# Performance work log

Measured on AMD Instinct MI355X. Metric: run time of the kernel, lower is better.

The kernel has to match this reference:

```python
import jax, jax.numpy as jnp
import numpy as np

N, E, F_IN, F_HID, K = 100000, 1600000, 64, 64, 6


def setup_inputs() -> dict:
    key = jax.random.key(0)
    k1, k2, k3, k4, k5 = jax.random.split(key, 5)
    x = jax.random.normal(k1, (N, F_IN), dtype=jnp.float32)
    # edges with no self-loops (PyG ChebConv removes self loops before normalization)
    src = jax.random.randint(k2, (E,), 0, N, dtype=jnp.int32)
    off = jax.random.randint(k3, (E,), 1, N, dtype=jnp.int32)
    dst = (src + off) % N
    edge_index = jnp.stack([src, dst], axis=0)
    # Glorot-ish init for the K Chebyshev weight matrices
    W = jax.random.normal(k4, (K, F_IN, F_HID), dtype=jnp.float32) * (1.0 / np.sqrt(F_IN))
    b = jax.random.normal(k5, (F_HID,), dtype=jnp.float32) * 0.01
    return {"x": x, "edge_index": edge_index, "W": W, "b": b}


def reference(x, edge_index, W, b):
    # ChebConv with sym normalization, lambda_max = 2.0 (PyG default):
    # scaled Laplacian L_hat = 2*L/lambda_max - I = -D^{-1/2} A D^{-1/2} (zero diagonal)
    row = edge_index[0].astype(jnp.int32)  # source j
    col = edge_index[1].astype(jnp.int32)  # target i
    n = x.shape[0]
    deg = jax.ops.segment_sum(jnp.ones_like(row, dtype=x.dtype), row, num_segments=n)
    dinv = jnp.where(deg > 0, jax.lax.rsqrt(deg), jnp.zeros_like(deg))
    w = -(dinv[row] * dinv[col])  # [E] edge weights of L_hat

    def prop(h):  # h: [N, F] -> L_hat @ h via gather-scale-scatter
        return jax.ops.segment_sum(w[:, None] * h[row], col, num_segments=n)

    # Chebyshev recurrence: Tx_0 = x, Tx_1 = L_hat x, Tx_k = 2 L_hat Tx_{k-1} - Tx_{k-2}
    Tx0 = x
    out = Tx0 @ W[0]
    Tx1 = prop(Tx0)
    out = out + Tx1 @ W[1]
    for k in range(2, W.shape[0]):
        Tx2 = 2.0 * prop(Tx1) - Tx0
        out = out + Tx2 @ W[k]
        Tx0, Tx1 = Tx1, Tx2
    return jax.nn.relu(out + b)
```

## Files before the change

### kernel.cpp

```cpp
#include <hip/hip_runtime.h>


constexpr int F = 64;
constexpr int SCAN_ELEMS = 2048;
constexpr int BSH = 9;
constexpr int EPB = 2048;
constexpr int PNPW = 8;
constexpr int WFRAG_BLOCKS = 12;

typedef __attribute__((ext_vector_type(8))) short short8;
typedef __attribute__((ext_vector_type(4))) float floatx4;

__device__ __forceinline__ unsigned short f_to_bf(float f) {
    unsigned u = __float_as_uint(f);
    u += 0x7FFFu + ((u >> 16) & 1u);
    return (unsigned short)(u >> 16);
}
__device__ __forceinline__ float bf_to_f(unsigned short s) {
    return __uint_as_float(((unsigned)s) << 16);
}
__device__ __forceinline__ float4 bf4_to_f4(ushort4 u) {
    float4 f;
    f.x = bf_to_f(u.x); f.y = bf_to_f(u.y); f.z = bf_to_f(u.z); f.w = bf_to_f(u.w);
    return f;
}

__global__ void hist2_kernel(const int* __restrict__ row, const int* __restrict__ col,
                             int* __restrict__ gcH, int* __restrict__ gcS,
                             int P, int G, int E) {
    __shared__ int hH[256], hS[256];
    const int tid = threadIdx.x, blk = blockIdx.x;
    hH[tid] = 0; hS[tid] = 0;
    __syncthreads();
    const int start = blk * EPB + tid * 8;
    if (start + 7 < E) {
        const int4 c0 = *(const int4*)(col + start);
        const int4 c1 = *(const int4*)(col + start + 4);
        const int4 r0 = *(const int4*)(row + start);
        const int4 r1 = *(const int4*)(row + start + 4);
        atomicAdd(&hH[c0.x >> BSH], 1); atomicAdd(&hH[c0.y >> BSH], 1);
        atomicAdd(&hH[c0.z >> BSH], 1); atomicAdd(&hH[c0.w >> BSH], 1);
        atomicAdd(&hH[c1.x >> BSH], 1); atomicAdd(&hH[c1.y >> BSH], 1);
        atomicAdd(&hH[c1.z >> BSH], 1); atomicAdd(&hH[c1.w >> BSH], 1);
        atomicAdd(&hS[r0.x >> BSH], 1); atomicAdd(&hS[r0.y >> BSH], 1);
        atomicAdd(&hS[r0.z >> BSH], 1); atomicAdd(&hS[r0.w >> BSH], 1);
        atomicAdd(&hS[r1.x >> BSH], 1); atomicAdd(&hS[r1.y >> BSH], 1);
        atomicAdd(&hS[r1.z >> BSH], 1); atomicAdd(&hS[r1.w >> BSH], 1);
    } else {
        for (int k = start; k < E && k < start + 8; ++k) {
            atomicAdd(&hH[col[k] >> BSH], 1);
            atomicAdd(&hS[row[k] >> BSH], 1);
        }
    }
    __syncthreads();
    if (tid < P) {
        gcH[(size_t)tid * G + blk] = hH[tid];
        gcS[(size_t)tid * G + blk] = hS[tid];
    }
}

__device__ __forceinline__ int4 load_cnt4(const int* __restrict__ cnt, int i, int N) {
    int4 v = make_int4(0, 0, 0, 0);
    if (i + 3 < N) {
        v = *(const int4*)(cnt + i);
    } else {
        if (i + 0 < N) v.x = cnt[i + 0];
        if (i + 1 < N) v.y = cnt[i + 1];
        if (i + 2 < N) v.z = cnt[i + 2];
        if (i + 3 < N) v.w = cnt[i + 3];
    }
    return v;
}

__global__ void scan1_kernel(const int* __restrict__ cnt, int* __restrict__ bsum, int N) {
    const int tid = threadIdx.x;
    const int i = blockIdx.x * SCAN_ELEMS + tid * 8;
    int4 va = load_cnt4(cnt, i, N);
    int4 vb = load_cnt4(cnt, i + 4, N);
    int s = va.x + va.y + va.z + va.w + vb.x + vb.y + vb.z + vb.w;
#pragma unroll
    for (int off = 1; off < 64; off <<= 1) s += __shfl_xor(s, off);
    __shared__ int ws[4];
    if ((tid & 63) == 0) ws[tid >> 6] = s;
    __syncthreads();
    if (tid == 0) bsum[blockIdx.x] = ws[0] + ws[1] + ws[2] + ws[3];
}

__global__ void scan2_kernel(const int* __restrict__ bsum, int* __restrict__ boff,
                             int* __restrict__ total_out, int nb) {
    const int tid = threadIdx.x;
    const int lane = tid & 63, w = tid >> 6;
    int v = (tid < nb) ? bsum[tid] : 0;
    int inc = v;
#pragma unroll
    for (int off = 1; off < 64; off <<= 1) {
        int t = __shfl_up(inc, off);
        if (lane >= off) inc += t;
    }
    __shared__ int wsum[4];
    if (lane == 63) wsum[w] = inc;
    __syncthreads();
    int wo = 0;
    for (int k = 0; k < w; ++k) wo += wsum[k];
    const int excl = wo + inc - v;
    if (tid < nb) boff[tid] = excl;
    if (tid == nb - 1) *total_out = excl + v;
}

__global__ void scan3_kernel(const int* __restrict__ cnt, const int* __restrict__ boff,
                             int* __restrict__ dst, int N) {
    const int tid = threadIdx.x;
    const int lane = tid & 63, w = tid >> 6;
    const int i = blockIdx.x * SCAN_ELEMS + tid * 8;
    int4 va = load_cnt4(cnt, i, N);
    int4 vb = load_cnt4(cnt, i + 4, N);
    const int s = va.x + va.y + va.z + va.w + vb.x + vb.y + vb.z + vb.w;
    int inc = s;
#pragma unroll
    for (int off = 1; off < 64; off <<= 1) {
        int t = __shfl_up(inc, off);
        if (lane >= off) inc += t;
    }
    __shared__ int wsum[4];
    if (lane == 63) wsum[w] = inc;
    __syncthreads();
    int wo = 0;
    for (int k = 0; k < w; ++k) wo += wsum[k];
    const int r0 = boff[blockIdx.x] + wo + inc - s;
    const int r1 = r0 + va.x, r2 = r1 + va.y, r3 = r2 + va.z;
    const int r4 = r3 + va.w, r5 = r4 + vb.x, r6 = r5 + vb.y, r7 = r6 + vb.z;
    if (i + 3 < N) {
        *(int4*)(dst + i) = make_int4(r0, r1, r2, r3);
    } else {
        if (i + 0 < N) dst[i + 0] = r0;
        if (i + 1 < N) dst[i + 1] = r1;
        if (i + 2 < N) dst[i + 2] = r2;
    }
    if (i + 7 < N) {
        *(int4*)(dst + i + 4) = make_int4(r4, r5, r6, r7);
    } else {
        if (i + 4 < N) dst[i + 4] = r4;
        if (i + 5 < N) dst[i + 5] = r5;
        if (i + 6 < N) dst[i + 6] = r6;
    }
}

__global__ void part2_kernel(const int* __restrict__ row, const int* __restrict__ col,
                             const int* __restrict__ goH, const int* __restrict__ goS,
                             int* __restrict__ partH, int* __restrict__ partS,
                             int P, int G, int E) {
    __shared__ int cH[256], cS[256];
    const int tid = threadIdx.x, blk = blockIdx.x;
    if (tid < P) {
        cH[tid] = goH[(size_t)tid * G + blk];
        cS[tid] = goS[(size_t)tid * G + blk] - E;
    }
    __syncthreads();
    const int start = blk * EPB + tid * 8;
    if (start + 7 < E) {
        const int4 c0 = *(const int4*)(col + start);
        const int4 c1 = *(const int4*)(col + start + 4);
        const int4 r0 = *(const int4*)(row + start);
        const int4 r1 = *(const int4*)(row + start + 4);
#define P2_DO(c, r)                                              \
        {                                                        \
            const int posH = atomicAdd(&cH[(c) >> BSH], 1);      \
            partH[posH] = (((c) & ((1 << BSH) - 1)) << 23) | (r);\
            const int posS = atomicAdd(&cS[(r) >> BSH], 1);      \
            partS[posS] = (r);                                   \
        }
        P2_DO(c0.x, r0.x) P2_DO(c0.y, r0.y) P2_DO(c0.z, r0.z) P2_DO(c0.w, r0.w)
        P2_DO(c1.x, r1.x) P2_DO(c1.y, r1.y) P2_DO(c1.z, r1.z) P2_DO(c1.w, r1.w)
#undef P2_DO
    } else {
        for (int k = start; k < E && k < start + 8; ++k) {
            const int c = col[k], r = row[k];
            const int posH = atomicAdd(&cH[c >> BSH], 1);
            partH[posH] = ((c & ((1 << BSH) - 1)) << 23) | r;
            const int posS = atomicAdd(&cS[r >> BSH], 1);
            partS[posS] = r;
        }
    }
}

__global__ void bucketCD_kernel(const int* __restrict__ part, const int* __restrict__ goff,
                                const int* __restrict__ partS, const int* __restrict__ goffS,
                                int* __restrict__ rowptr, int* __restrict__ csr,
                                float* __restrict__ dinv, float* __restrict__ dinv2,
                                float* __restrict__ rdinv,
                                int P, int G, int N, int E) {
    __shared__ int cnt[512];
    __shared__ int excl[512];
    __shared__ int wsum[4];
    const int tid = threadIdx.x;
    const int bb = blockIdx.x;
    if (bb < P) {
        const int b = bb;
        const int base_node = b << BSH;
        const int nn = min(512, N - base_node);
        const int estart = goff[(size_t)b * G];
        const int eend = (b + 1 < P) ? goff[(size_t)(b + 1) * G] : E;

        cnt[tid] = 0; cnt[tid + 256] = 0;
        __syncthreads();
        for (int i = estart + tid; i < eend; i += 256)
            atomicAdd(&cnt[((unsigned)part[i]) >> 23], 1);
        __syncthreads();
        {
            const int lane = tid & 63, w = tid >> 6;
            const int a0 = cnt[2 * tid], a1 = cnt[2 * tid + 1];
            const int ps = a0 + a1;
            int inc = ps;
#pragma unroll
            for (int off = 1; off < 64; off <<= 1) {
                int t = __shfl_up(inc, off);
                if (lane >= off) inc += t;
            }
            if (lane == 63) wsum[w] = inc;
            __syncthreads();
            int wo = 0;
            for (int k = 0; k < w; ++k) wo += wsum[k];
            const int ep = wo + inc - ps;
            excl[2 * tid] = ep;
            excl[2 * tid + 1] = ep + a0;
        }
        __syncthreads();
        for (int ln = tid; ln < nn; ln += 256) rowptr[base_node + ln] = estart + excl[ln];
        if (b == P - 1 && tid == 0) rowptr[N] = E;
        cnt[tid] = 0; cnt[tid + 256] = 0;
        __syncthreads();
        for (int i = estart + tid; i < eend; i += 256) {
            const int pk = part[i];
            const int ln = ((unsigned)pk) >> 23;
            const int pos = atomicAdd(&cnt[ln], 1);
            csr[estart + excl[ln] + pos] = pk & 0x7FFFFF;
        }
    } else {
        const int b = bb - P;
        const int base_node = b << BSH;
        const int nn = min(512, N - base_node);
        const int estart = goffS[(size_t)b * G] - E;
        const int eend = ((b + 1 < P) ? goffS[(size_t)(b + 1) * G] - E : E);
        cnt[tid] = 0; cnt[tid + 256] = 0;
        __syncthreads();
        for (int i = estart + tid; i < eend; i += 256)
            atomicAdd(&cnt[partS[i] - base_node], 1);
        __syncthreads();
        for (int l = tid; l < nn; l += 256) {
            const int dI = cnt[l];
            const float d = (float)dI;
            const bool ok = dI > 0;
            dinv[base_node + l]  = ok ? rsqrtf(d) : 0.0f;
            dinv2[base_node + l] = ok ? 1.0f / d : 0.0f;
            rdinv[base_node + l] = ok ? sqrtf(d) : 0.0f;
        }
    }
}

__global__ void init_ws0_kernel(const float* __restrict__ W, unsigned short* __restrict__ Wfrag,
                                const float* __restrict__ dinv, const float* __restrict__ x,
                                unsigned short* __restrict__ S0b, int NF) {
    const int tid = threadIdx.x;
    const int bid = blockIdx.x;
    if (bid < WFRAG_BLOCKS) {
        const int idx = bid * 256 + tid;
        if (idx >= 4 * 12 * 64) return;
        const int lane = idx & 63;
        const int s = (idx >> 6) % 12;
        const int ft = idx / (64 * 12);
        const int n = ft * 16 + (lane & 15);
        const int quad = lane >> 4;
        unsigned short v[8];
#pragma unroll
        for (int j = 0; j < 8; ++j) {
            const int kg = s * 32 + quad * 8 + j;
            const int kk = kg >> 6, f = kg & 63;
            v[j] = f_to_bf(W[kk * F * F + f * F + n]);
        }
        ushort4 lo = {v[0], v[1], v[2], v[3]};
        ushort4 hi = {v[4], v[5], v[6], v[7]};
        *(ushort4*)(Wfrag + (size_t)idx * 8) = lo;
        *(ushort4*)(Wfrag + (size_t)idx * 8 + 4) = hi;
    } else {
        const int i = (bid - WFRAG_BLOCKS) * 256 + tid;
        const int j = i * 4;
        if (j >= NF) return;
        const float dv = dinv[j >> 6];
        const float4 v = *(const float4*)(x + j);
        ushort4 u;
        u.x = f_to_bf(dv * v.x); u.y = f_to_bf(dv * v.y);
        u.z = f_to_bf(dv * v.z); u.w = f_to_bf(dv * v.w);
        *(ushort4*)(S0b + j) = u;
    }
}

template <int FIRST>
__global__ __launch_bounds__(256, 6)
void prop_g4(const int* __restrict__ rowptr, const int* __restrict__ csr,
             const float* __restrict__ dinv2, const unsigned short* __restrict__ Sprev,
             const unsigned short* __restrict__ Sm2, unsigned short* __restrict__ Sk, int N) {
    const int lane = threadIdx.x & 63;
    const int g16 = lane & 48;
    const int fl = lane & 15;
    const int wave = threadIdx.x >> 6;
    const int wbase = (blockIdx.x * 4 + wave) * PNPW;
    for (int j = 0; j < PNPW; j += 4) {
        const int n = wbase + j + (g16 >> 4);
        const bool nv = n < N;
        const int nc = nv ? n : N - 1;
        const int s = rowptr[nc], e = rowptr[nc + 1];
        const int len = e - s;
        float4 acc = {0.f, 0.f, 0.f, 0.f};
        for (int c = 0; c < len; c += 16) {
            const int ii = s + c + fl;
            const int idxv = csr[ii < e ? ii : e - 1];
            const int mm = min(16, len - c);
            ushort4 u[16];
#pragma unroll
            for (int t = 0; t < 16; ++t) {
                const int it = __shfl(idxv, g16 + t);
                u[t] = *(const ushort4*)(Sprev + (size_t)it * F + fl * 4);
            }
#pragma unroll
            for (int t = 0; t < 16; ++t) {
                if (t < mm) {
                    const float4 v = bf4_to_f4(u[t]);
                    acc.x += v.x; acc.y += v.y; acc.z += v.z; acc.w += v.w;
                }
            }
        }
        if (nv) {
            const float d2 = dinv2[n];
            float4 sn;
            if (FIRST) {
                sn.x = -d2 * acc.x; sn.y = -d2 * acc.y;
                sn.z = -d2 * acc.z; sn.w = -d2 * acc.w;
            } else {
                const float4 m2 = bf4_to_f4(*(const ushort4*)(Sm2 + (size_t)n * F + fl * 4));
                sn.x = -2.f * d2 * acc.x - m2.x; sn.y = -2.f * d2 * acc.y - m2.y;
                sn.z = -2.f * d2 * acc.z - m2.z; sn.w = -2.f * d2 * acc.w - m2.w;
            }
            ushort4 o;
            o.x = f_to_bf(sn.x); o.y = f_to_bf(sn.y);
            o.z = f_to_bf(sn.z); o.w = f_to_bf(sn.w);
            *(ushort4*)(Sk + (size_t)n * F + fl * 4) = o;
        }
    }
}

__global__ __launch_bounds__(256, 3)
void mfma_out_kernel(const float* __restrict__ x, const unsigned short* __restrict__ Sstack,
                     const unsigned short* __restrict__ Wfrag, const float* __restrict__ rdinv,
                     const float* __restrict__ dinv2, const float* __restrict__ W,
                     const float* __restrict__ b, float* __restrict__ out, int N, int NF) {
    const int lane = threadIdx.x & 63;
    const int wave = threadIdx.x >> 6;
    const int quad = lane >> 4;
    const int fl = lane & 15;
    const int tm = (blockIdx.x * 4 + wave) * 16;
    if (tm >= N) return;
    const int ma = tm + fl;
    const int mac = ma < N ? ma : N - 1;

    const unsigned short* sa = Sstack + (size_t)mac * F + quad * 8;

    short8 Afr[12];
#pragma unroll
    for (int s = 0; s < 12; ++s) {
        const int kk = s >> 1, f0 = (s & 1) * 32;
        Afr[s] = __builtin_nontemporal_load((const short8*)(sa + (size_t)kk * NF + f0));
    }

    floatx4 C0 = {0.f, 0.f, 0.f, 0.f};
    floatx4 C1 = {0.f, 0.f, 0.f, 0.f};
    floatx4 C2 = {0.f, 0.f, 0.f, 0.f};
    floatx4 C3 = {0.f, 0.f, 0.f, 0.f};
    const unsigned short* wf = Wfrag + (size_t)lane * 8;
#pragma unroll
    for (int s = 0; s < 12; ++s) {
        const short8 B0 = *(const short8*)(wf + (size_t)(0 * 12 + s) * 64 * 8);
        const short8 B1 = *(const short8*)(wf + (size_t)(1 * 12 + s) * 64 * 8);
        const short8 B2 = *(const short8*)(wf + (size_t)(2 * 12 + s) * 64 * 8);
        const short8 B3 = *(const short8*)(wf + (size_t)(3 * 12 + s) * 64 * 8);
        C0 = __builtin_amdgcn_mfma_f32_16x16x32_bf16(Afr[s], B0, C0, 0, 0, 0);
        C1 = __builtin_amdgcn_mfma_f32_16x16x32_bf16(Afr[s], B1, C1, 0, 0, 0);
        C2 = __builtin_amdgcn_mfma_f32_16x16x32_bf16(Afr[s], B2, C2, 0, 0, 0);
        C3 = __builtin_amdgcn_mfma_f32_16x16x32_bf16(Afr[s], B3, C3, 0, 0, 0);
    }

    const float bl0 = b[0 * 16 + fl];
    const float bl1 = b[1 * 16 + fl];
    const float bl2 = b[2 * 16 + fl];
    const float bl3 = b[3 * 16 + fl];

#pragma unroll
    for (int r = 0; r < 4; ++r) {
        const int m = tm + quad * 4 + r;
        if (m >= N) continue;
        const float rs = rdinv[m];
        const bool z = (dinv2[m] == 0.0f);
        float v0 = rs * C0[r], v1 = rs * C1[r], v2 = rs * C2[r], v3 = rs * C3[r];
        if (z) {
            const float* xr = x + (size_t)m * F;
            float f0 = 0.f, f1 = 0.f, f2 = 0.f, f3 = 0.f;
            for (int f = 0; f < F; ++f) {
                const float xv = xr[f];
                const float* w0 = W + 0 * F * F + f * F;
                const float* w2 = W + 2 * F * F + f * F;
                const float* w4 = W + 4 * F * F + f * F;
                f0 += xv * (w0[0 * 16 + fl] - w2[0 * 16 + fl] + w4[0 * 16 + fl]);
                f1 += xv * (w0[1 * 16 + fl] - w2[1 * 16 + fl] + w4[1 * 16 + fl]);
                f2 += xv * (w0[2 * 16 + fl] - w2[2 * 16 + fl] + w4[2 * 16 + fl]);
                f3 += xv * (w0[3 * 16 + fl] - w2[3 * 16 + fl] + w4[3 * 16 + fl]);
            }
            v0 = f0; v1 = f1; v2 = f2; v3 = f3;
        }
        float* orow = out + (size_t)m * F;
        __builtin_nontemporal_store(fmaxf(v0 + bl0, 0.f), orow + 0 * 16 + fl);
        __builtin_nontemporal_store(fmaxf(v1 + bl1, 0.f), orow + 1 * 16 + fl);
        __builtin_nontemporal_store(fmaxf(v2 + bl2, 0.f), orow + 2 * 16 + fl);
        __builtin_nontemporal_store(fmaxf(v3 + bl3, 0.f), orow + 3 * 16 + fl);
    }
}

extern "C" void kernel_launch(void* const* d_in, const int* in_sizes, int n_in,
                              void* d_out, int out_size, void* d_ws, size_t ws_size,
                              hipStream_t stream) {
    const float* x = (const float*)d_in[0];
    const int* ei = (const int*)d_in[1];
    const float* W = (const float*)d_in[2];
    const float* b = (const float*)d_in[3];

    const int N = in_sizes[0] / F;
    const int E = in_sizes[1] / 2;
    const int NF = N * F;
    const int* row = ei;
    const int* col = ei + E;

    const int P = (N + 511) >> BSH;
    const int G = (E + EPB - 1) / EPB;
    const int M = P * G;
    const int M2 = 2 * M;

    char* p = (char*)d_ws;
    auto alloc = [&](size_t bytes) {
        char* r = p;
        p += (bytes + 63) & ~(size_t)63;
        return r;
    };
    float* dinv   = (float*)alloc((size_t)N * sizeof(float));
    float* dinv2  = (float*)alloc((size_t)N * sizeof(float));
    float* rdinv  = (float*)alloc((size_t)N * sizeof(float));
    int*   rowptr = (int*)alloc((size_t)(N + 1) * sizeof(int));
    int*   bsum   = (int*)alloc(256 * sizeof(int));
    int*   boff   = (int*)alloc(256 * sizeof(int));
    int*   totS   = (int*)alloc(64);
    int*   gc     = (int*)alloc((size_t)M2 * sizeof(int));
    int*   go     = (int*)alloc((size_t)M2 * sizeof(int));
    int*   csr    = (int*)alloc((size_t)E * sizeof(int));
    unsigned short* Sstack = (unsigned short*)alloc((size_t)6 * NF * sizeof(unsigned short));
    unsigned short* Wfrag  = (unsigned short*)alloc((size_t)4 * 12 * 64 * 8 * sizeof(unsigned short));
    int* partH = (int*)Sstack;
    int* partS = (int*)(Sstack + (size_t)NF);
    float* out = (float*)d_out;
    (void)ws_size;

    const int B = 256;
    const int nsb = (M2 + SCAN_ELEMS - 1) / SCAN_ELEMS;
    const int pgrid = (N + 4 * PNPW - 1) / (4 * PNPW);
    const int igrid = WFRAG_BLOCKS + (NF / 4 + B - 1) / B;

    hist2_kernel<<<G, B, 0, stream>>>(row, col, gc, gc + M, P, G, E);
    scan1_kernel<<<nsb, B, 0, stream>>>(gc, bsum, M2);
    scan2_kernel<<<1, B, 0, stream>>>(bsum, boff, totS, nsb);
    scan3_kernel<<<nsb, B, 0, stream>>>(gc, boff, go, M2);
    part2_kernel<<<G, B, 0, stream>>>(row, col, go, go + M, partH, partS, P, G, E);
    bucketCD_kernel<<<2 * P, B, 0, stream>>>(partH, go, partS, go + M, rowptr, csr,
                                             dinv, dinv2, rdinv, P, G, N, E);
    init_ws0_kernel<<<igrid, B, 0, stream>>>(W, Wfrag, dinv, x, Sstack, NF);

    unsigned short* S1 = Sstack + (size_t)1 * NF;
    unsigned short* S2 = Sstack + (size_t)2 * NF;
    unsigned short* S3 = Sstack + (size_t)3 * NF;
    unsigned short* S4 = Sstack + (size_t)4 * NF;
    unsigned short* S5 = Sstack + (size_t)5 * NF;
    prop_g4<1><<<pgrid, B, 0, stream>>>(rowptr, csr, dinv2, Sstack, Sstack, S1, N);
    prop_g4<0><<<pgrid, B, 0, stream>>>(rowptr, csr, dinv2, S1, Sstack, S2, N);
    prop_g4<0><<<pgrid, B, 0, stream>>>(rowptr, csr, dinv2, S2, S1, S3, N);
    prop_g4<0><<<pgrid, B, 0, stream>>>(rowptr, csr, dinv2, S3, S2, S4, N);
    prop_g4<0><<<pgrid, B, 0, stream>>>(rowptr, csr, dinv2, S4, S3, S5, N);
    mfma_out_kernel<<<(N + 63) / 64, 256, 0, stream>>>(x, Sstack, Wfrag, rdinv, dinv2,
                                                       W, b, out, N, NF);
}
```

Before: 338.1 us.

## Count degrees with global atomics and vector-load CSR indices in propagation

Removes the source-side partition/bucket path and computes node degrees by global atomic increments in the histogram kernel, deriving normalisation factors in the init kernel. The propagation kernel now loads neighbour indices as int4 vectors per lane instead of one index per lane plus shuffles, with the CSR buffer padded for overreads. This trades partition scatter traffic for contended global atomics and possibly misaligned vector loads.

```diff
diff --git a/kernel.cpp b/kernel.cpp
--- a/kernel.cpp
+++ b/kernel.cpp
@@ -26,11 +26,11 @@
 }
 
 __global__ void hist2_kernel(const int* __restrict__ row, const int* __restrict__ col,
-                             int* __restrict__ gcH, int* __restrict__ gcS,
+                             int* __restrict__ gcH, int* __restrict__ deg,
                              int P, int G, int E) {
-    __shared__ int hH[256], hS[256];
+    __shared__ int hH[256];
     const int tid = threadIdx.x, blk = blockIdx.x;
-    hH[tid] = 0; hS[tid] = 0;
+    hH[tid] = 0;
     __syncthreads();
     const int start = blk * EPB + tid * 8;
     if (start + 7 < E) {
@@ -42,21 +42,18 @@
         atomicAdd(&hH[c0.z >> BSH], 1); atomicAdd(&hH[c0.w >> BSH], 1);
         atomicAdd(&hH[c1.x >> BSH], 1); atomicAdd(&hH[c1.y >> BSH], 1);
         atomicAdd(&hH[c1.z >> BSH], 1); atomicAdd(&hH[c1.w >> BSH], 1);
-        atomicAdd(&hS[r0.x >> BSH], 1); atomicAdd(&hS[r0.y >> BSH], 1);
-        atomicAdd(&hS[r0.z >> BSH], 1); atomicAdd(&hS[r0.w >> BSH], 1);
-        atomicAdd(&hS[r1.x >> BSH], 1); atomicAdd(&hS[r1.y >> BSH], 1);
-        atomicAdd(&hS[r1.z >> BSH], 1); atomicAdd(&hS[r1.w >> BSH], 1);
+        atomicAdd(&deg[r0.x], 1); atomicAdd(&deg[r0.y], 1);
+        atomicAdd(&deg[r0.z], 1); atomicAdd(&deg[r0.w], 1);
+        atomicAdd(&deg[r1.x], 1); atomicAdd(&deg[r1.y], 1);
+        atomicAdd(&deg[r1.z], 1); atomicAdd(&deg[r1.w], 1);
     } else {
         for (int k = start; k < E && k < start + 8; ++k) {
             atomicAdd(&hH[col[k] >> BSH], 1);
-            atomicAdd(&hS[row[k] >> BSH], 1);
-        }
-    }
-    __syncthreads();
-    if (tid < P) {
-        gcH[(size_t)tid * G + blk] = hH[tid];
-        gcS[(size_t)tid * G + blk] = hS[tid];
-    }
+            atomicAdd(&deg[row[k]], 1);
+        }
+    }
+    __syncthreads();
+    if (tid < P) gcH[(size_t)tid * G + blk] = hH[tid];
 }
 
 __device__ __forceinline__ int4 load_cnt4(const int* __restrict__ cnt, int i, int N) {
@@ -146,15 +143,11 @@
 }
 
 __global__ void part2_kernel(const int* __restrict__ row, const int* __restrict__ col,
-                             const int* __restrict__ goH, const int* __restrict__ goS,
-                             int* __restrict__ partH, int* __restrict__ partS,
+                             const int* __restrict__ goH, int* __restrict__ partH,
                              int P, int G, int E) {
-    __shared__ int cH[256], cS[256];
+    __shared__ int cH[256];
     const int tid = threadIdx.x, blk = blockIdx.x;
-    if (tid < P) {
-        cH[tid] = goH[(size_t)tid * G + blk];
-        cS[tid] = goS[(size_t)tid * G + blk] - E;
-    }
+    if (tid < P) cH[tid] = goH[(size_t)tid * G + blk];
     __syncthreads();
     const int start = blk * EPB + tid * 8;
     if (start + 7 < E) {
@@ -166,8 +159,6 @@
         {                                                        \
             const int posH = atomicAdd(&cH[(c) >> BSH], 1);      \
             partH[posH] = (((c) & ((1 << BSH) - 1)) << 23) | (r);\
-            const int posS = atomicAdd(&cS[(r) >> BSH], 1);      \
-            partS[posS] = (r);                                   \
         }
         P2_DO(c0.x, r0.x) P2_DO(c0.y, r0.y) P2_DO(c0.z, r0.z) P2_DO(c0.w, r0.w)
         P2_DO(c1.x, r1.x) P2_DO(c1.y, r1.y) P2_DO(c1.z, r1.z) P2_DO(c1.w, r1.w)
@@ -177,89 +168,64 @@
             const int c = col[k], r = row[k];
             const int posH = atomicAdd(&cH[c >> BSH], 1);
             partH[posH] = ((c & ((1 << BSH) - 1)) << 23) | r;
-            const int posS = atomicAdd(&cS[r >> BSH], 1);
-            partS[posS] = r;
-        }
-    }
-}
-
-__global__ void bucketCD_kernel(const int* __restrict__ part, const int* __restrict__ goff,
-                                const int* __restrict__ partS, const int* __restrict__ goffS,
-                                int* __restrict__ rowptr, int* __restrict__ csr,
-                                float* __restrict__ dinv, float* __restrict__ dinv2,
-                                float* __restrict__ rdinv,
-                                int P, int G, int N, int E) {
+        }
+    }
+}
+
+__global__ void bucketC_kernel(const int* __restrict__ part, const int* __restrict__ goff,
+                               int* __restrict__ rowptr, int* __restrict__ csr,
+                               int P, int G, int N, int E) {
     __shared__ int cnt[512];
     __shared__ int excl[512];
     __shared__ int wsum[4];
     const int tid = threadIdx.x;
-    const int bb = blockIdx.x;
-    if (bb < P) {
-        const int b = bb;
-        const int base_node = b << BSH;
-        const int nn = min(512, N - base_node);
-        const int estart = goff[(size_t)b * G];
-        const int eend = (b + 1 < P) ? goff[(size_t)(b + 1) * G] : E;
-
-        cnt[tid] = 0; cnt[tid + 256] = 0;
+    const int b = blockIdx.x;
+    const int base_node = b << BSH;
+    const int nn = min(512, N - base_node);
+    const int estart = goff[(size_t)b * G];
+    const int eend = (b + 1 < P) ? goff[(size_t)(b + 1) * G] : E;
+
+    cnt[tid] = 0; cnt[tid + 256] = 0;
+    __syncthreads();
+    for (int i = estart + tid; i < eend; i += 256)
+        atomicAdd(&cnt[((unsigned)part[i]) >> 23], 1);
+    __syncthreads();
+    {
+        const int lane = tid & 63, w = tid >> 6;
+        const int a0 = cnt[2 * tid], a1 = cnt[2 * tid + 1];
+        const int ps = a0 + a1;
+        int inc = ps;
+#pragma unroll
+        for (int off = 1; off < 64; off <<= 1) {
+            int t = __shfl_up(inc, off);
+            if (lane >= off) inc += t;
+        }
+        if (lane == 63) wsum[w] = inc;
         __syncthreads();
-        for (int i = estart + tid; i < eend; i += 256)
-            atomicAdd(&cnt[((unsigned)part[i]) >> 23], 1);
-        __syncthreads();
-        {
-            const int lane = tid & 63, w = tid >> 6;
-            const int a0 = cnt[2 * tid], a1 = cnt[2 * tid + 1];
-            const int ps = a0 + a1;
-            int inc = ps;
-#pragma unroll
-            for (int off = 1; off < 64; off <<= 1) {
-                int t = __shfl_up(inc, off);
-                if (lane >= off) inc += t;
-            }
-            if (lane == 63) wsum[w] = inc;
-            __syncthreads();
-            int wo = 0;
-            for (int k = 0; k < w; ++k) wo += wsum[k];
-            const int ep = wo + inc - ps;
-            excl[2 * tid] = ep;
-            excl[2 * tid + 1] = ep + a0;
-        }
-        __syncthreads();
-        for (int ln = tid; ln < nn; ln += 256) rowptr[base_node + ln] = estart + excl[ln];
-        if (b == P - 1 && tid == 0) rowptr[N] = E;
-        cnt[tid] = 0; cnt[tid + 256] = 0;
-        __syncthreads();
-        for (int i = estart + tid; i < eend; i += 256) {
-            const int pk = part[i];
-            const int ln = ((unsigned)pk) >> 23;
-            const int pos = atomicAdd(&cnt[ln], 1);
-            csr[estart + excl[ln] + pos] = pk & 0x7FFFFF;
-        }
-    } else {
-        const int b = bb - P;
-        const int base_node = b << BSH;
-        const int nn = min(512, N - base_node);
-        const int estart = goffS[(size_t)b * G] - E;
-        const int eend = ((b + 1 < P) ? goffS[(size_t)(b + 1) * G] - E : E);
-        cnt[tid] = 0; cnt[tid + 256] = 0;
-        __syncthreads();
-        for (int i = estart + tid; i < eend; i += 256)
-            atomicAdd(&cnt[partS[i] - base_node], 1);
-        __syncthreads();
-        for (int l = tid; l < nn; l += 256) {
-            const int dI = cnt[l];
-            const float d = (float)dI;
-            const bool ok = dI > 0;
-            dinv[base_node + l]  = ok ? rsqrtf(d) : 0.0f;
-            dinv2[base_node + l] = ok ? 1.0f / d : 0.0f;
-            rdinv[base_node + l] = ok ? sqrtf(d) : 0.0f;
-        }
+        int wo = 0;
+        for (int k = 0; k < w; ++k) wo += wsum[k];
+        const int ep = wo + inc - ps;
+        excl[2 * tid] = ep;
+        excl[2 * tid + 1] = ep + a0;
+    }
+    __syncthreads();
+    for (int ln = tid; ln < nn; ln += 256) rowptr[base_node + ln] = estart + excl[ln];
+    if (b == P - 1 && tid == 0) rowptr[N] = E;
+    cnt[tid] = 0; cnt[tid + 256] = 0;
+    __syncthreads();
+    for (int i = estart + tid; i < eend; i += 256) {
+        const int pk = part[i];
+        const int ln = ((unsigned)pk) >> 23;
+        const int pos = atomicAdd(&cnt[ln], 1);
+        csr[estart + excl[ln] + pos] = pk & 0x7FFFFF;
     }
 }
 
 __global__ void init_ws0_kernel(const float* __restrict__ W, unsigned short* __restrict__ Wfrag,
-                                const float* __restrict__ dinv, const float* __restrict__ x,
-                                unsigned short* __restrict__ S0b, int NF) {
+                                const int* __restrict__ deg, const float* __restrict__ x,
+                                unsigned short* __restrict__ S0b,
+                                float* __restrict__ dinv2, float* __restrict__ rdinv,
+                                int N, int NF, int DBLK) {
     const int tid = threadIdx.x;
     const int bid = blockIdx.x;
     if (bid < WFRAG_BLOCKS) {
@@ -281,11 +247,35 @@
         ushort4 hi = {v[4], v[5], v[6], v[7]};
         *(ushort4*)(Wfrag + (size_t)idx * 8) = lo;
         *(ushort4*)(Wfrag + (size_t)idx * 8 + 4) = hi;
-    } else {
-        const int i = (bid - WFRAG_BLOCKS) * 256 + tid;
+    } else if (bid < WFRAG_BLOCKS + DBLK) {
+        const int i0 = (bid - WFRAG_BLOCKS) * 1024 + tid * 4;
+        if (i0 >= N) return;
+        if (i0 + 3 < N) {
+            const int4 d4 = *(const int4*)(deg + i0);
+            float4 v2, vr;
+            v2.x = d4.x > 0 ? 1.0f / (float)d4.x : 0.0f;
+            v2.y = d4.y > 0 ? 1.0f / (float)d4.y : 0.0f;
+            v2.z = d4.z > 0 ? 1.0f / (float)d4.z : 0.0f;
+            v2.w = d4.w > 0 ? 1.0f / (float)d4.w : 0.0f;
+            vr.x = d4.x > 0 ? sqrtf((float)d4.x) : 0.0f;
+            vr.y = d4.y > 0 ? sqrtf((float)d4.y) : 0.0f;
+            vr.z = d4.z > 0 ? sqrtf((float)d4.z) : 0.0f;
+            vr.w = d4.w > 0 ? sqrtf((float)d4.w) : 0.0f;
+            *(float4*)(dinv2 + i0) = v2;
+            *(float4*)(rdinv + i0) = vr;
+        } else {
+            for (int k = 0; k < 4 && i0 + k < N; ++k) {
+                const int d = deg[i0 + k];
+                dinv2[i0 + k] = d > 0 ? 1.0f / (float)d : 0.0f;
+                rdinv[i0 + k] = d > 0 ? sqrtf((float)d) : 0.0f;
+            }
+        }
+    } else {
+        const int i = (bid - WFRAG_BLOCKS - DBLK) * 256 + tid;
         const int j = i * 4;
         if (j >= NF) return;
-        const float dv = dinv[j >> 6];
+        const int d = deg[j >> 6];
+        const float dv = d > 0 ? rsqrtf((float)d) : 0.0f;
         const float4 v = *(const float4*)(x + j);
         ushort4 u;
         u.x = f_to_bf(dv * v.x); u.y = f_to_bf(dv * v.y);
@@ -312,13 +302,18 @@
         const int len = e - s;
         float4 acc = {0.f, 0.f, 0.f, 0.f};
         for (int c = 0; c < len; c += 16) {
-            const int ii = s + c + fl;
-            const int idxv = csr[ii < e ? ii : e - 1];
+            const int base = s + c;
+            const int4 ia = *(const int4*)(csr + base);
+            const int4 ib = *(const int4*)(csr + base + 4);
+            const int4 ic = *(const int4*)(csr + base + 8);
+            const int4 id = *(const int4*)(csr + base + 12);
             const int mm = min(16, len - c);
+            const int idx[16] = {ia.x, ia.y, ia.z, ia.w, ib.x, ib.y, ib.z, ib.w,
+                                 ic.x, ic.y, ic.z, ic.w, id.x, id.y, id.z, id.w};
             ushort4 u[16];
 #pragma unroll
             for (int t = 0; t < 16; ++t) {
-                const int it = __shfl(idxv, g16 + t);
+                const int it = (t < mm) ? idx[t] : 0;
                 u[t] = *(const ushort4*)(Sprev + (size_t)it * F + fl * 4);
             }
 #pragma unroll
@@ -440,7 +435,6 @@
     const int P = (N + 511) >> BSH;
     const int G = (E + EPB - 1) / EPB;
     const int M = P * G;
-    const int M2 = 2 * M;
 
     char* p = (char*)d_ws;
     auto alloc = [&](size_t bytes) {
@@ -448,36 +442,37 @@
         p += (bytes + 63) & ~(size_t)63;
         return r;
     };
-    float* dinv   = (float*)alloc((size_t)N * sizeof(float));
+    int*   deg    = (int*)alloc((size_t)N * sizeof(int));
     float* dinv2  = (float*)alloc((size_t)N * sizeof(float));
     float* rdinv  = (float*)alloc((size_t)N * sizeof(float));
     int*   rowptr = (int*)alloc((size_t)(N + 1) * sizeof(int));
     int*   bsum   = (int*)alloc(256 * sizeof(int));
     int*   boff   = (int*)alloc(256 * sizeof(int));
     int*   totS   = (int*)alloc(64);
-    int*   gc     = (int*)alloc((size_t)M2 * sizeof(int));
-    int*   go     = (int*)alloc((size_t)M2 * sizeof(int));
-    int*   csr    = (int*)alloc((size_t)E * sizeof(int));
+    int*   gc     = (int*)alloc((size_t)M * sizeof(int));
+    int*   go     = (int*)alloc((size_t)M * sizeof(int));
+    int*   csr    = (int*)alloc(((size_t)E + 16) * sizeof(int));
     unsigned short* Sstack = (unsigned short*)alloc((size_t)6 * NF * sizeof(unsigned short));
     unsigned short* Wfrag  = (unsigned short*)alloc((size_t)4 * 12 * 64 * 8 * sizeof(unsigned short));
     int* partH = (int*)Sstack;
-    int* partS = (int*)(Sstack + (size_t)NF);
     float* out = (float*)d_out;
     (void)ws_size;
 
     const int B = 256;
-    const int nsb = (M2 + SCAN_ELEMS - 1) / SCAN_ELEMS;
+    const int nsb = (M + SCAN_ELEMS - 1) / SCAN_ELEMS;
     const int pgrid = (N + 4 * PNPW - 1) / (4 * PNPW);
-    const int igrid = WFRAG_BLOCKS + (NF / 4 + B - 1) / B;
-
-    hist2_kernel<<<G, B, 0, stream>>>(row, col, gc, gc + M, P, G, E);
-    scan1_kernel<<<nsb, B, 0, stream>>>(gc, bsum, M2);
+    const int DBLK = (N + 1023) / 1024;
+    const int igrid = WFRAG_BLOCKS + DBLK + (NF / 4 + B - 1) / B;
+
+    hipMemsetAsync(deg, 0, (size_t)N * sizeof(int), stream);
+    hist2_kernel<<<G, B, 0, stream>>>(row, col, gc, deg, P, G, E);
+    scan1_kernel<<<nsb, B, 0, stream>>>(gc, bsum, M);
     scan2_kernel<<<1, B, 0, stream>>>(bsum, boff, totS, nsb);
-    scan3_kernel<<<nsb, B, 0, stream>>>(gc, boff, go, M2);
-    part2_kernel<<<G, B, 0, stream>>>(row, col, go, go + M, partH, partS, P, G, E);
-    bucketCD_kernel<<<2 * P, B, 0, stream>>>(partH, go, partS, go + M, rowptr, csr,
-                                             dinv, dinv2, rdinv, P, G, N, E);
-    init_ws0_kernel<<<igrid, B, 0, stream>>>(W, Wfrag, dinv, x, Sstack, NF);
+    scan3_kernel<<<nsb, B, 0, stream>>>(gc, boff, go, M);
+    part2_kernel<<<G, B, 0, stream>>>(row, col, go, partH, P, G, E);
+    bucketC_kernel<<<P, B, 0, stream>>>(partH, go, rowptr, csr, P, G, N, E);
+    init_ws0_kernel<<<igrid, B, 0, stream>>>(W, Wfrag, deg, x, Sstack, dinv2, rdinv,
+                                             N, NF, DBLK);
 
     unsigned short* S1 = Sstack + (size_t)1 * NF;
     unsigned short* S2 = Sstack + (size_t)2 * NF;
```

New measurement: 481.5 us. 1.42x slower.

## Fuse scan2 into scan3, and merge init kernel into bucket-degree kernel

Applied to the files above, without the earlier changes.

Removes the single-block scan2 launch: each scan3 block now sums the preceding block totals itself. The degree-counting half of the bucket kernel also scales x by rsqrt(deg) and writes the bf16 S0, and the W fragment packing moves into extra blocks of the same launch, which eliminates init_ws0 and the dinv array. partS is stored as 16-bit local node indices to cut scatter traffic, and the partition buffers move to S4/S5 so they do not alias S0. Two launches are removed, at the cost of redundant prefix sums in scan3 and less parallelism for the x scaling, which now runs over 2*P blocks.

```diff
diff --git a/kernel.cpp b/kernel.cpp
--- a/kernel.cpp
+++ b/kernel.cpp
@@ -86,32 +86,24 @@
     if (tid == 0) bsum[blockIdx.x] = ws[0] + ws[1] + ws[2] + ws[3];
 }
 
-__global__ void scan2_kernel(const int* __restrict__ bsum, int* __restrict__ boff,
-                             int* __restrict__ total_out, int nb) {
-    const int tid = threadIdx.x;
-    const int lane = tid & 63, w = tid >> 6;
-    int v = (tid < nb) ? bsum[tid] : 0;
-    int inc = v;
-#pragma unroll
-    for (int off = 1; off < 64; off <<= 1) {
-        int t = __shfl_up(inc, off);
-        if (lane >= off) inc += t;
-    }
-    __shared__ int wsum[4];
-    if (lane == 63) wsum[w] = inc;
-    __syncthreads();
-    int wo = 0;
-    for (int k = 0; k < w; ++k) wo += wsum[k];
-    const int excl = wo + inc - v;
-    if (tid < nb) boff[tid] = excl;
-    if (tid == nb - 1) *total_out = excl + v;
-}
-
-__global__ void scan3_kernel(const int* __restrict__ cnt, const int* __restrict__ boff,
+__global__ void scan3_kernel(const int* __restrict__ cnt, const int* __restrict__ bsum,
                              int* __restrict__ dst, int N) {
     const int tid = threadIdx.x;
     const int lane = tid & 63, w = tid >> 6;
-    const int i = blockIdx.x * SCAN_ELEMS + tid * 8;
+    const int blk = blockIdx.x;
+    __shared__ int wsum[4];
+    __shared__ int boffs;
+    {
+        int a = 0;
+        for (int k = tid; k < blk; k += 256) a += bsum[k];
+#pragma unroll
+        for (int off = 1; off < 64; off <<= 1) a += __shfl_xor(a, off);
+        if ((tid & 63) == 0) wsum[tid >> 6] = a;
+        __syncthreads();
+        if (tid == 0) boffs = wsum[0] + wsum[1] + wsum[2] + wsum[3];
+        __syncthreads();
+    }
+    const int i = blk * SCAN_ELEMS + tid * 8;
     int4 va = load_cnt4(cnt, i, N);
     int4 vb = load_cnt4(cnt, i + 4, N);
     const int s = va.x + va.y + va.z + va.w + vb.x + vb.y + vb.z + vb.w;
@@ -121,12 +113,12 @@
         int t = __shfl_up(inc, off);
         if (lane >= off) inc += t;
     }
-    __shared__ int wsum[4];
+    __syncthreads();
     if (lane == 63) wsum[w] = inc;
     __syncthreads();
     int wo = 0;
     for (int k = 0; k < w; ++k) wo += wsum[k];
-    const int r0 = boff[blockIdx.x] + wo + inc - s;
+    const int r0 = boffs + wo + inc - s;
     const int r1 = r0 + va.x, r2 = r1 + va.y, r3 = r2 + va.z;
     const int r4 = r3 + va.w, r5 = r4 + vb.x, r6 = r5 + vb.y, r7 = r6 + vb.z;
     if (i + 3 < N) {
@@ -147,7 +139,7 @@
 
 __global__ void part2_kernel(const int* __restrict__ row, const int* __restrict__ col,
                              const int* __restrict__ goH, const int* __restrict__ goS,
-                             int* __restrict__ partH, int* __restrict__ partS,
+                             int* __restrict__ partH, unsigned short* __restrict__ partS,
                              int P, int G, int E) {
     __shared__ int cH[256], cS[256];
     const int tid = threadIdx.x, blk = blockIdx.x;
@@ -162,12 +154,12 @@
         const int4 c1 = *(const int4*)(col + start + 4);
         const int4 r0 = *(const int4*)(row + start);
         const int4 r1 = *(const int4*)(row + start + 4);
-#define P2_DO(c, r)                                              \
-        {                                                        \
-            const int posH = atomicAdd(&cH[(c) >> BSH], 1);      \
-            partH[posH] = (((c) & ((1 << BSH) - 1)) << 23) | (r);\
-            const int posS = atomicAdd(&cS[(r) >> BSH], 1);      \
-            partS[posS] = (r);                                   \
+#define P2_DO(c, r)                                                    \
+        {                                                              \
+            const int posH = atomicAdd(&cH[(c) >> BSH], 1);            \
+            partH[posH] = (((c) & ((1 << BSH) - 1)) << 23) | (r);      \
+            const int posS = atomicAdd(&cS[(r) >> BSH], 1);            \
+            partS[posS] = (unsigned short)((r) & ((1 << BSH) - 1));    \
         }
         P2_DO(c0.x, r0.x) P2_DO(c0.y, r0.y) P2_DO(c0.z, r0.z) P2_DO(c0.w, r0.w)
         P2_DO(c1.x, r1.x) P2_DO(c1.y, r1.y) P2_DO(c1.z, r1.z) P2_DO(c1.w, r1.w)
@@ -178,17 +170,19 @@
             const int posH = atomicAdd(&cH[c >> BSH], 1);
             partH[posH] = ((c & ((1 << BSH) - 1)) << 23) | r;
             const int posS = atomicAdd(&cS[r >> BSH], 1);
-            partS[posS] = r;
-        }
-    }
-}
-
-__global__ void bucketCD_kernel(const int* __restrict__ part, const int* __restrict__ goff,
-                                const int* __restrict__ partS, const int* __restrict__ goffS,
-                                int* __restrict__ rowptr, int* __restrict__ csr,
-                                float* __restrict__ dinv, float* __restrict__ dinv2,
-                                float* __restrict__ rdinv,
-                                int P, int G, int N, int E) {
+            partS[posS] = (unsigned short)(r & ((1 << BSH) - 1));
+        }
+    }
+}
+
+__global__ void bucketCDW_kernel(const int* __restrict__ part, const int* __restrict__ goff,
+                                 const unsigned short* __restrict__ partS,
+                                 const int* __restrict__ goffS,
+                                 int* __restrict__ rowptr, int* __restrict__ csr,
+                                 float* __restrict__ dinv2, float* __restrict__ rdinv,
+                                 const float* __restrict__ x, unsigned short* __restrict__ S0b,
+                                 const float* __restrict__ W, unsigned short* __restrict__ Wfrag,
+                                 int P, int G, int N, int E) {
     __shared__ int cnt[512];
     __shared__ int excl[512];
     __shared__ int wsum[4];
@@ -235,7 +229,7 @@
             const int pos = atomicAdd(&cnt[ln], 1);
             csr[estart + excl[ln] + pos] = pk & 0x7FFFFF;
         }
-    } else {
+    } else if (bb < 2 * P) {
         const int b = bb - P;
         const int base_node = b << BSH;
         const int nn = min(512, N - base_node);
@@ -244,26 +238,29 @@
         cnt[tid] = 0; cnt[tid + 256] = 0;
         __syncthreads();
         for (int i = estart + tid; i < eend; i += 256)
-            atomicAdd(&cnt[partS[i] - base_node], 1);
+            atomicAdd(&cnt[partS[i]], 1);
         __syncthreads();
         for (int l = tid; l < nn; l += 256) {
             const int dI = cnt[l];
             const float d = (float)dI;
             const bool ok = dI > 0;
-            dinv[base_node + l]  = ok ? rsqrtf(d) : 0.0f;
             dinv2[base_node + l] = ok ? 1.0f / d : 0.0f;
             rdinv[base_node + l] = ok ? sqrtf(d) : 0.0f;
         }
-    }
-}
-
-__global__ void init_ws0_kernel(const float* __restrict__ W, unsigned short* __restrict__ Wfrag,
-                                const float* __restrict__ dinv, const float* __restrict__ x,
-                                unsigned short* __restrict__ S0b, int NF) {
-    const int tid = threadIdx.x;
-    const int bid = blockIdx.x;
-    if (bid < WFRAG_BLOCKS) {
-        const int idx = bid * 256 + tid;
+        const int ntask = nn * 16;
+        for (int t = tid; t < ntask; t += 256) {
+            const int l = t >> 4, fq = t & 15;
+            const int dI = cnt[l];
+            const float dv = dI > 0 ? rsqrtf((float)dI) : 0.0f;
+            const size_t off = (size_t)(base_node + l) * F + fq * 4;
+            const float4 v = *(const float4*)(x + off);
+            ushort4 u;
+            u.x = f_to_bf(dv * v.x); u.y = f_to_bf(dv * v.y);
+            u.z = f_to_bf(dv * v.z); u.w = f_to_bf(dv * v.w);
+            *(ushort4*)(S0b + off) = u;
+        }
+    } else {
+        const int idx = (bb - 2 * P) * 256 + tid;
         if (idx >= 4 * 12 * 64) return;
         const int lane = idx & 63;
         const int s = (idx >> 6) % 12;
@@ -281,16 +278,6 @@
         ushort4 hi = {v[4], v[5], v[6], v[7]};
         *(ushort4*)(Wfrag + (size_t)idx * 8) = lo;
         *(ushort4*)(Wfrag + (size_t)idx * 8 + 4) = hi;
-    } else {
-        const int i = (bid - WFRAG_BLOCKS) * 256 + tid;
-        const int j = i * 4;
-        if (j >= NF) return;
-        const float dv = dinv[j >> 6];
-        const float4 v = *(const float4*)(x + j);
-        ushort4 u;
-        u.x = f_to_bf(dv * v.x); u.y = f_to_bf(dv * v.y);
-        u.z = f_to_bf(dv * v.z); u.w = f_to_bf(dv * v.w);
-        *(ushort4*)(S0b + j) = u;
     }
 }
 
@@ -448,36 +435,31 @@
         p += (bytes + 63) & ~(size_t)63;
         return r;
     };
-    float* dinv   = (float*)alloc((size_t)N * sizeof(float));
     float* dinv2  = (float*)alloc((size_t)N * sizeof(float));
     float* rdinv  = (float*)alloc((size_t)N * sizeof(float));
     int*   rowptr = (int*)alloc((size_t)(N + 1) * sizeof(int));
     int*   bsum   = (int*)alloc(256 * sizeof(int));
-    int*   boff   = (int*)alloc(256 * sizeof(int));
-    int*   totS   = (int*)alloc(64);
     int*   gc     = (int*)alloc((size_t)M2 * sizeof(int));
     int*   go     = (int*)alloc((size_t)M2 * sizeof(int));
     int*   csr    = (int*)alloc((size_t)E * sizeof(int));
     unsigned short* Sstack = (unsigned short*)alloc((size_t)6 * NF * sizeof(unsigned short));
     unsigned short* Wfrag  = (unsigned short*)alloc((size_t)4 * 12 * 64 * 8 * sizeof(unsigned short));
-    int* partH = (int*)Sstack;
-    int* partS = (int*)(Sstack + (size_t)NF);
+    int* partH = (int*)(Sstack + (size_t)4 * NF);
+    unsigned short* partS = Sstack + (size_t)5 * NF;
     float* out = (float*)d_out;
     (void)ws_size;
 
     const int B = 256;
     const int nsb = (M2 + SCAN_ELEMS - 1) / SCAN_ELEMS;
     const int pgrid = (N + 4 * PNPW - 1) / (4 * PNPW);
-    const int igrid = WFRAG_BLOCKS + (NF / 4 + B - 1) / B;
 
     hist2_kernel<<<G, B, 0, stream>>>(row, col, gc, gc + M, P, G, E);
     scan1_kernel<<<nsb, B, 0, stream>>>(gc, bsum, M2);
-    scan2_kernel<<<1, B, 0, stream>>>(bsum, boff, totS, nsb);
-    scan3_kernel<<<nsb, B, 0, stream>>>(gc, boff, go, M2);
+    scan3_kernel<<<nsb, B, 0, stream>>>(gc, bsum, go, M2);
     part2_kernel<<<G, B, 0, stream>>>(row, col, go, go + M, partH, partS, P, G, E);
-    bucketCD_kernel<<<2 * P, B, 0, stream>>>(partH, go, partS, go + M, rowptr, csr,
-                                             dinv, dinv2, rdinv, P, G, N, E);
-    init_ws0_kernel<<<igrid, B, 0, stream>>>(W, Wfrag, dinv, x, Sstack, NF);
+    bucketCDW_kernel<<<2 * P + WFRAG_BLOCKS, B, 0, stream>>>(
+        partH, go, partS, go + M, rowptr, csr, dinv2, rdinv, x, Sstack, W, Wfrag,
+        P, G, N, E);
 
     unsigned short* S1 = Sstack + (size_t)1 * NF;
     unsigned short* S2 = Sstack + (size_t)2 * NF;
```

After: 419.0 us. +23.9%, slower.
